# Kernel optimization log

Measured on AMD Instinct MI355X. Metric: run time of the kernel, lower is better.

The kernel has to match this reference:

```python
import jax, jax.numpy as jnp
import numpy as np

N_ELEMS = 200000
N_REACTIONS = 100000
ELEM_DIM = 200
REACT_DIM = 128
N_HEADS = 3
DIMS = [ELEM_DIM + REACT_DIM, 256, 256, 256, 256, 128, 128, 64]  # ResidualNetwork layer dims


def _init(key, shape, fan_in):
    return jax.random.normal(key, shape, dtype=jnp.float32) * (1.0 / np.sqrt(fan_in))


def setup_inputs() -> dict:
    key = jax.random.key(0)
    ks = jax.random.split(key, 32)
    H = N_HEADS
    inp = {
        "orig_elem_fea": jax.random.normal(ks[0], (N_ELEMS, ELEM_DIM), dtype=jnp.float32),
        "reaction_elem_idx": jax.random.randint(ks[1], (N_ELEMS,), 0, N_REACTIONS, dtype=jnp.int32),
        "reaction_embed": jax.random.normal(ks[2], (N_REACTIONS, REACT_DIM), dtype=jnp.float32),
    }
    k = 3
    for i in range(7):
        inp[f"fcW{i}"] = _init(ks[k], (H, DIMS[i], DIMS[i + 1]), DIMS[i]); k += 1
        inp[f"fcb{i}"] = jnp.zeros((H, DIMS[i + 1]), dtype=jnp.float32)
    # residual projections only where in_dim != out_dim (layers 0, 4, 6)
    for i in (0, 4, 6):
        inp[f"resW{i}"] = _init(ks[k], (H, DIMS[i], DIMS[i + 1]), DIMS[i]); k += 1
    inp["outW"] = _init(ks[k], (H, DIMS[-1], 1), DIMS[-1]); k += 1
    inp["outb"] = jnp.zeros((H, 1), dtype=jnp.float32)
    return inp


def reference(orig_elem_fea, reaction_elem_idx, reaction_embed,
              fcW0, fcb0, fcW1, fcb1, fcW2, fcb2, fcW3, fcb3,
              fcW4, fcb4, fcW5, fcb5, fcW6, fcb6,
              resW0, resW4, resW6, outW, outb):
    C = reaction_embed.shape[0]
    idx = reaction_elem_idx
    # gather reaction embedding per elem and concat: (N, E+R)
    fea = jnp.concatenate([orig_elem_fea, reaction_embed[idx]], axis=1)
    # per-head ResidualNetwork gate: h axis = head
    h = jax.nn.relu(jnp.einsum('nf,hfo->hno', fea, fcW0) + fcb0[:, None, :]) \
        + jnp.einsum('nf,hfo->hno', fea, resW0)
    for W, b in ((fcW1, fcb1), (fcW2, fcb2), (fcW3, fcb3)):
        h = jax.nn.relu(jnp.einsum('hnf,hfo->hno', h, W) + b[:, None, :]) + h
    h = jax.nn.relu(jnp.einsum('hnf,hfo->hno', h, fcW4) + fcb4[:, None, :]) \
        + jnp.einsum('hnf,hfo->hno', h, resW4)
    h = jax.nn.relu(jnp.einsum('hnf,hfo->hno', h, fcW5) + fcb5[:, None, :]) + h
    h = jax.nn.relu(jnp.einsum('hnf,hfo->hno', h, fcW6) + fcb6[:, None, :]) \
        + jnp.einsum('hnf,hfo->hno', h, resW6)
    gate = (jnp.einsum('hnf,hfo->hno', h, outW) + outb[:, None, :])[..., 0]  # (H, N)
    # segment softmax over reactions, per head
    seg_max = jax.vmap(lambda g: jax.ops.segment_max(g, idx, num_segments=C))(gate)
    gate = jnp.exp(gate - seg_max[:, idx])
    seg_sum = jax.vmap(lambda g: jax.ops.segment_sum(g, idx, num_segments=C))(gate)
    gate = gate / (seg_sum[:, idx] + 1e-13)
    return jnp.mean(gate, axis=0)  # (N,) normalised stoichiometries
```

## Files before the change

kernel.cpp:

```cpp
#include <hip/hip_runtime.h>

#define NELEM  200000
#define NREACT 100000
#define EDIM   200
#define RDIM   128
#define F0     328
#define F0PAD  352
#define NH     3
#define MT     64
#define NT     256
#define SA     360

typedef _Float16 f16x8 __attribute__((ext_vector_type(8)));
typedef _Float16 f16x4 __attribute__((ext_vector_type(4)));
typedef float    f32x4 __attribute__((ext_vector_type(4)));

struct WSeg { const float* src; _Float16* dst; int K, N, Kpad, nb; };
struct WTab { WSeg s[10]; };

__global__ void wconv_all(WTab t)
{
    __shared__ float sT[64 * 33];
    int b = blockIdx.x;
    for (int i = 0; i < 10; ++i) {
        if (b < t.s[i].nb) {
            const WSeg g = t.s[i];
            const int ntn = 3 * g.N / 64;
            const int tn = b % ntn, tk = b / ntn;
            const int col = tn * 64;
            const int h = col / g.N, n0 = col - h * g.N;
            const int k0 = tk * 32;
            const int tid = threadIdx.x;

            const int nl = tid & 63;
            for (int kk = tid >> 6; kk < 32; kk += 4) {
                const int k = k0 + kk;
                float v = (k < g.K) ? g.src[((size_t)h * g.K + k) * g.N + n0 + nl] : 0.f;
                sT[nl * 33 + kk] = v;
            }
            __syncthreads();

            const int kl = tid & 31;
            for (int nn = tid >> 5; nn < 64; nn += 8)
                g.dst[(size_t)(col + nn) * g.Kpad + k0 + kl] = (_Float16)sT[nn * 33 + kl];
            return;
        }
        b -= t.s[i].nb;
    }
}

template<int TN>
__device__ __forceinline__ void pin_step_refill()
{
    if constexpr (TN == 4) {
#pragma unroll
        for (int g = 0; g < 4; ++g) {
            __builtin_amdgcn_sched_group_barrier(0x008, 2, 0);
            __builtin_amdgcn_sched_group_barrier(0x020, 1, 0);
            __builtin_amdgcn_sched_group_barrier(0x008, 2, 0);
            __builtin_amdgcn_sched_group_barrier(0x100, 1, 0);
        }
    } else if constexpr (TN == 2) {
#pragma unroll
        for (int g = 0; g < 2; ++g) {
            __builtin_amdgcn_sched_group_barrier(0x008, 2, 0);
            __builtin_amdgcn_sched_group_barrier(0x020, 1, 0);
            __builtin_amdgcn_sched_group_barrier(0x008, 2, 0);
            __builtin_amdgcn_sched_group_barrier(0x100, 2, 0);
        }
    } else {
        __builtin_amdgcn_sched_group_barrier(0x008, 2, 0);
        __builtin_amdgcn_sched_group_barrier(0x020, 1, 0);
        __builtin_amdgcn_sched_group_barrier(0x008, 2, 0);
        __builtin_amdgcn_sched_group_barrier(0x100, 4, 0);
    }
}

template<int N>
__device__ __forceinline__ void pin_step_mfma_only()
{
    __builtin_amdgcn_sched_group_barrier(0x008, N, 0);
}

template<int TN, int KSTEPS, int KPAD>
__device__ __forceinline__ void gemm_pass(
    const _Float16* __restrict__ buf,
    const _Float16* __restrict__ w,
    f32x4 (&acc)[4][TN], int n0, int r, int q)
{
    const _Float16* aBase = buf + r * SA + q * 8;
    const _Float16* wBase = w + ((size_t)n0 + r) * KPAD + q * 8;

    f16x8 a0[4], a1[4], b0[TN], b1[TN];
#pragma unroll
    for (int nt = 0; nt < TN; ++nt) b0[nt] = *(const f16x8*)(wBase + (size_t)nt * 16 * KPAD);
#pragma unroll
    for (int mt = 0; mt < 4; ++mt) a0[mt] = *(const f16x8*)(aBase + mt * 16 * SA);
#pragma unroll
    for (int nt = 0; nt < TN; ++nt) b1[nt] = *(const f16x8*)(wBase + (size_t)nt * 16 * KPAD + 32);
#pragma unroll
    for (int mt = 0; mt < 4; ++mt) a1[mt] = *(const f16x8*)(aBase + mt * 16 * SA + 32);

#pragma unroll
    for (int kt = 0; kt < KSTEPS; kt += 2) {
#pragma unroll
        for (int nt = 0; nt < TN; ++nt)
#pragma unroll
            for (int mt = 0; mt < 4; ++mt)
                acc[mt][nt] = __builtin_amdgcn_mfma_f32_16x16x32_f16(b0[nt], a0[mt], acc[mt][nt], 0, 0, 0);
        if (kt + 2 < KSTEPS) {
#pragma unroll
            for (int nt = 0; nt < TN; ++nt)
                b0[nt] = *(const f16x8*)(wBase + (size_t)nt * 16 * KPAD + (kt + 2) * 32);
#pragma unroll
            for (int mt = 0; mt < 4; ++mt)
                a0[mt] = *(const f16x8*)(aBase + mt * 16 * SA + (kt + 2) * 32);
            pin_step_refill<TN>();
        } else {
            pin_step_mfma_only<4 * TN>();
        }
        if (kt + 1 < KSTEPS) {
#pragma unroll
            for (int nt = 0; nt < TN; ++nt)
#pragma unroll
                for (int mt = 0; mt < 4; ++mt)
                    acc[mt][nt] = __builtin_amdgcn_mfma_f32_16x16x32_f16(b1[nt], a1[mt], acc[mt][nt], 0, 0, 0);
            if (kt + 3 < KSTEPS) {
#pragma unroll
                for (int nt = 0; nt < TN; ++nt)
                    b1[nt] = *(const f16x8*)(wBase + (size_t)nt * 16 * KPAD + (kt + 3) * 32);
#pragma unroll
                for (int mt = 0; mt < 4; ++mt)
                    a1[mt] = *(const f16x8*)(aBase + mt * 16 * SA + (kt + 3) * 32);
                pin_step_refill<TN>();
            } else {
                pin_step_mfma_only<4 * TN>();
            }
        }
    }
}

template<int TN, int KSTEPS, int KPAD>
__device__ __forceinline__ void layer_id(
    _Float16* __restrict__ buf,
    const _Float16* __restrict__ wFc,
    const float* __restrict__ bias, int n0, int lane)
{
    const int r = lane & 15, q = lane >> 4;
    f32x4 acc[4][TN];
#pragma unroll
    for (int mt = 0; mt < 4; ++mt)
#pragma unroll
        for (int nt = 0; nt < TN; ++nt) acc[mt][nt] = (f32x4){0.f, 0.f, 0.f, 0.f};

    gemm_pass<TN, KSTEPS, KPAD>(buf, wFc, acc, n0, r, q);

    __syncthreads();

#pragma unroll
    for (int nt = 0; nt < TN; ++nt) {
        const int colb = n0 + nt * 16 + q * 4;
        const f32x4 bv = *(const f32x4*)(bias + colb);
#pragma unroll
        for (int mt = 0; mt < 4; ++mt) {
            _Float16* p = buf + (mt * 16 + r) * SA + colb;
            f16x4 o = *(const f16x4*)p;
            f16x4 z;
#pragma unroll
            for (int i = 0; i < 4; ++i)
                z[i] = (_Float16)(fmaxf(acc[mt][nt][i] + bv[i], 0.f) + (float)o[i]);
            *(f16x4*)p = z;
        }
    }
    __syncthreads();
}

template<int TN, int KSTEPS, int KPAD>
__device__ __forceinline__ void layer_proj(
    _Float16* __restrict__ buf,
    const _Float16* __restrict__ wFc, const _Float16* __restrict__ wRes,
    const float* __restrict__ bias, int n0, int lane)
{
    const int r = lane & 15, q = lane >> 4;
    f32x4 acc[4][TN];
#pragma unroll
    for (int mt = 0; mt < 4; ++mt)
#pragma unroll
        for (int nt = 0; nt < TN; ++nt) acc[mt][nt] = (f32x4){0.f, 0.f, 0.f, 0.f};

    gemm_pass<TN, KSTEPS, KPAD>(buf, wFc, acc, n0, r, q);

#pragma unroll
    for (int nt = 0; nt < TN; ++nt) {
        const f32x4 bv = *(const f32x4*)(bias + n0 + nt * 16 + q * 4);
#pragma unroll
        for (int mt = 0; mt < 4; ++mt)
#pragma unroll
            for (int i = 0; i < 4; ++i)
                acc[mt][nt][i] = fmaxf(acc[mt][nt][i] + bv[i], 0.f);
    }

    gemm_pass<TN, KSTEPS, KPAD>(buf, wRes, acc, n0, r, q);

    __syncthreads();

#pragma unroll
    for (int nt = 0; nt < TN; ++nt) {
        const int colb = n0 + nt * 16 + q * 4;
#pragma unroll
        for (int mt = 0; mt < 4; ++mt) {
            f16x4 z;
#pragma unroll
            for (int i = 0; i < 4; ++i) z[i] = (_Float16)acc[mt][nt][i];
            *(f16x4*)(buf + (mt * 16 + r) * SA + colb) = z;
        }
    }
    __syncthreads();
}

__global__ __launch_bounds__(NT, 3)
void mlp_mfma(const float* __restrict__ elem, const int* __restrict__ ridx,
              const float* __restrict__ embed,
              const _Float16* __restrict__ wb,
              const float* __restrict__ fcb0, const float* __restrict__ fcb1,
              const float* __restrict__ fcb2, const float* __restrict__ fcb3,
              const float* __restrict__ fcb4, const float* __restrict__ fcb5,
              const float* __restrict__ fcb6,
              const float* __restrict__ outW, const float* __restrict__ outb,
              float* __restrict__ gate, unsigned int* __restrict__ segmax)
{
    __shared__ __align__(16) _Float16 sX[MT * SA];
    __shared__ int sidx[MT];

    const int tid = threadIdx.x, lane = tid & 63, wave = tid >> 6;
    const int head = blockIdx.y;
    const int row0 = blockIdx.x * MT;

    if (tid < MT) sidx[tid] = ridx[row0 + tid];
    __syncthreads();

    for (int rr = wave; rr < MT; rr += 4) {
        const float* es = elem + (size_t)(row0 + rr) * EDIM;
        const float* ms = embed + (size_t)sidx[rr] * RDIM;
        for (int c = lane; c < F0PAD / 4; c += 64) {
            f32x4 v;
            if (c < EDIM / 4)            v = *(const f32x4*)(es + 4 * c);
            else if (c < F0 / 4)         v = *(const f32x4*)(ms + 4 * c - EDIM);
            else                         v = (f32x4){0.f, 0.f, 0.f, 0.f};
            f16x4 hv;
#pragma unroll
            for (int i = 0; i < 4; ++i) hv[i] = (_Float16)v[i];
            *(f16x4*)(sX + rr * SA + 4 * c) = hv;
        }
    }
    __syncthreads();

    const size_t h = head;
    const int n64 = wave * 64, n32 = wave * 32, n16 = wave * 16;

    const _Float16* wt_fc0  = wb;
    const _Float16* wt_res0 = wb + 270336;
    const _Float16* wt_fc1  = wb + 540672;
    const _Float16* wt_fc2  = wb + 737280;
    const _Float16* wt_fc3  = wb + 933888;
    const _Float16* wt_fc4  = wb + 1130496;
    const _Float16* wt_res4 = wb + 1228800;
    const _Float16* wt_fc5  = wb + 1327104;
    const _Float16* wt_fc6  = wb + 1376256;
    const _Float16* wt_res6 = wb + 1400832;

    layer_proj<4, 11, 352>(sX, wt_fc0 + h * 90112, wt_res0 + h * 90112, fcb0 + h * 256, n64, lane);
    layer_id  <4, 8, 256>(sX, wt_fc1 + h * 65536, fcb1 + h * 256, n64, lane);
    layer_id  <4, 8, 256>(sX, wt_fc2 + h * 65536, fcb2 + h * 256, n64, lane);
    layer_id  <4, 8, 256>(sX, wt_fc3 + h * 65536, fcb3 + h * 256, n64, lane);
    layer_proj<2, 8, 256>(sX, wt_fc4 + h * 32768, wt_res4 + h * 32768, fcb4 + h * 128, n32, lane);
    layer_id  <2, 4, 128>(sX, wt_fc5 + h * 16384, fcb5 + h * 128, n32, lane);
    layer_proj<1, 4, 128>(sX, wt_fc6 + h * 8192,  wt_res6 + h * 8192,  fcb6 + h * 64,  n16, lane);

    if (tid < MT) {
        const _Float16* hv = sX + tid * SA;
        const float* wv = outW + h * 64;
        float g = outb[head];
#pragma unroll
        for (int j = 0; j < 8; ++j) {
            f16x8 hx = *(const f16x8*)(hv + j * 8);
#pragma unroll
            for (int i = 0; i < 8; ++i) g = fmaf((float)hx[i], wv[j * 8 + i], g);
        }
        gate[head * NELEM + row0 + tid] = g;
        unsigned int bits = __float_as_uint(g);
        unsigned int enc  = (bits & 0x80000000u) ? ~bits : (bits | 0x80000000u);
        atomicMax(&segmax[head * NREACT + sidx[tid]], enc);
    }
}

__global__ void phase2_kernel(float* __restrict__ gate, const int* __restrict__ ridx,
                              const unsigned int* __restrict__ segmax,
                              float* __restrict__ segsum)
{
    int i = blockIdx.x * blockDim.x + threadIdx.x;
    if (i >= NH * NELEM) return;
    int h = i / NELEM;
    int n = i - h * NELEM;
    int j = ridx[n];
    unsigned int enc  = segmax[h * NREACT + j];
    unsigned int bits = (enc & 0x80000000u) ? (enc & 0x7FFFFFFFu) : ~enc;
    float m = __uint_as_float(bits);
    float e = __expf(gate[i] - m);
    gate[i] = e;
    atomicAdd(&segsum[h * NREACT + j], e);
}

__global__ void phase3_kernel(const float* __restrict__ gate, const int* __restrict__ ridx,
                              const float* __restrict__ segsum, float* __restrict__ out)
{
    int n = blockIdx.x * blockDim.x + threadIdx.x;
    if (n >= NELEM) return;
    int j = ridx[n];
    float s = 0.0f;
#pragma unroll
    for (int h = 0; h < NH; ++h)
        s += gate[h * NELEM + n] / (segsum[h * NREACT + j] + 1e-13f);
    out[n] = s * (1.0f / 3.0f);
}

extern "C" void kernel_launch(void* const* d_in, const int* in_sizes, int n_in,
                              void* d_out, int out_size, void* d_ws, size_t ws_size,
                              hipStream_t stream)
{
    const float* elem  = (const float*)d_in[0];
    const int*   ridx  = (const int*)  d_in[1];
    const float* embed = (const float*)d_in[2];
    const float* fcW0  = (const float*)d_in[3];
    const float* fcb0  = (const float*)d_in[4];
    const float* fcW1  = (const float*)d_in[5];
    const float* fcb1  = (const float*)d_in[6];
    const float* fcW2  = (const float*)d_in[7];
    const float* fcb2  = (const float*)d_in[8];
    const float* fcW3  = (const float*)d_in[9];
    const float* fcb3  = (const float*)d_in[10];
    const float* fcW4  = (const float*)d_in[11];
    const float* fcb4  = (const float*)d_in[12];
    const float* fcW5  = (const float*)d_in[13];
    const float* fcb5  = (const float*)d_in[14];
    const float* fcW6  = (const float*)d_in[15];
    const float* fcb6  = (const float*)d_in[16];
    const float* resW0 = (const float*)d_in[17];
    const float* resW4 = (const float*)d_in[18];
    const float* resW6 = (const float*)d_in[19];
    const float* outW  = (const float*)d_in[20];
    const float* outb  = (const float*)d_in[21];

    float*        gate   = (float*)d_ws;
    unsigned int* segmax = (unsigned int*)d_ws + 600000;
    float*        segsum = (float*)d_ws + 900000;
    _Float16*     wbuf   = (_Float16*)((float*)d_ws + 1200000);

    hipMemsetAsync((void*)segmax, 0, sizeof(unsigned int) * 600000, stream);

    WTab t;
    t.s[0] = { fcW0,  wbuf,           328, 256, 352, 132 };
    t.s[1] = { resW0, wbuf + 270336,  328, 256, 352, 132 };
    t.s[2] = { fcW1,  wbuf + 540672,  256, 256, 256,  96 };
    t.s[3] = { fcW2,  wbuf + 737280,  256, 256, 256,  96 };
    t.s[4] = { fcW3,  wbuf + 933888,  256, 256, 256,  96 };
    t.s[5] = { fcW4,  wbuf + 1130496, 256, 128, 256,  48 };
    t.s[6] = { resW4, wbuf + 1228800, 256, 128, 256,  48 };
    t.s[7] = { fcW5,  wbuf + 1327104, 128, 128, 128,  24 };
    t.s[8] = { fcW6,  wbuf + 1376256, 128,  64, 128,  12 };
    t.s[9] = { resW6, wbuf + 1400832, 128,  64, 128,  12 };
    wconv_all<<<696, 256, 0, stream>>>(t);

    dim3 grid(NELEM / MT, NH);
    mlp_mfma<<<grid, NT, 0, stream>>>(elem, ridx, embed, wbuf,
                                      fcb0, fcb1, fcb2, fcb3, fcb4, fcb5, fcb6,
                                      outW, outb, gate, segmax);

    int tot = NH * NELEM;
    phase2_kernel<<<(tot + 255) / 256, 256, 0, stream>>>(gate, ridx, segmax, segsum);
    phase3_kernel<<<(NELEM + 255) / 256, 256, 0, stream>>>(gate, ridx, segsum, (float*)d_out);
}
```

Measured before the change: 1.361 ms.

## Use eight waves per block splitting output columns more finely

Doubles the block to 512 threads so each wave computes half as many output columns per layer (TN halved). The last 64-wide layer gates the extra waves off while keeping them at the block barriers. The aim is more waves resident per CU to hide load latency. In exchange, each A fragment read from LDS is reused across fewer MFMAs, so LDS traffic per FLOP roughly doubles, and the launch bounds now ask for 6 blocks of 512 threads, which tightens register limits.

```diff
diff --git a/kernel.cpp b/kernel.cpp
--- a/kernel.cpp
+++ b/kernel.cpp
@@ -8,7 +8,7 @@
 #define F0PAD  352
 #define NH     3
 #define MT     64
-#define NT     256
+#define NT     512
 #define SA     360
 
 typedef _Float16 f16x8 __attribute__((ext_vector_type(8)));
@@ -52,15 +52,7 @@
 template<int TN>
 __device__ __forceinline__ void pin_step_refill()
 {
-    if constexpr (TN == 4) {
-#pragma unroll
-        for (int g = 0; g < 4; ++g) {
-            __builtin_amdgcn_sched_group_barrier(0x008, 2, 0);
-            __builtin_amdgcn_sched_group_barrier(0x020, 1, 0);
-            __builtin_amdgcn_sched_group_barrier(0x008, 2, 0);
-            __builtin_amdgcn_sched_group_barrier(0x100, 1, 0);
-        }
-    } else if constexpr (TN == 2) {
+    if constexpr (TN == 2) {
 #pragma unroll
         for (int g = 0; g < 2; ++g) {
             __builtin_amdgcn_sched_group_barrier(0x008, 2, 0);
@@ -142,34 +134,37 @@
 
 template<int TN, int KSTEPS, int KPAD>
 __device__ __forceinline__ void layer_id(
-    _Float16* __restrict__ buf,
+    bool active, _Float16* __restrict__ buf,
     const _Float16* __restrict__ wFc,
     const float* __restrict__ bias, int n0, int lane)
 {
     const int r = lane & 15, q = lane >> 4;
     f32x4 acc[4][TN];
-#pragma unroll
-    for (int mt = 0; mt < 4; ++mt)
-#pragma unroll
-        for (int nt = 0; nt < TN; ++nt) acc[mt][nt] = (f32x4){0.f, 0.f, 0.f, 0.f};
-
-    gemm_pass<TN, KSTEPS, KPAD>(buf, wFc, acc, n0, r, q);
-
-    __syncthreads();
-
-#pragma unroll
-    for (int nt = 0; nt < TN; ++nt) {
-        const int colb = n0 + nt * 16 + q * 4;
-        const f32x4 bv = *(const f32x4*)(bias + colb);
-#pragma unroll
-        for (int mt = 0; mt < 4; ++mt) {
-            _Float16* p = buf + (mt * 16 + r) * SA + colb;
-            f16x4 o = *(const f16x4*)p;
-            f16x4 z;
-#pragma unroll
-            for (int i = 0; i < 4; ++i)
-                z[i] = (_Float16)(fmaxf(acc[mt][nt][i] + bv[i], 0.f) + (float)o[i]);
-            *(f16x4*)p = z;
+    if (active) {
+#pragma unroll
+        for (int mt = 0; mt < 4; ++mt)
+#pragma unroll
+            for (int nt = 0; nt < TN; ++nt) acc[mt][nt] = (f32x4){0.f, 0.f, 0.f, 0.f};
+        gemm_pass<TN, KSTEPS, KPAD>(buf, wFc, acc, n0, r, q);
+    }
+
+    __syncthreads();
+
+    if (active) {
+#pragma unroll
+        for (int nt = 0; nt < TN; ++nt) {
+            const int colb = n0 + nt * 16 + q * 4;
+            const f32x4 bv = *(const f32x4*)(bias + colb);
+#pragma unroll
+            for (int mt = 0; mt < 4; ++mt) {
+                _Float16* p = buf + (mt * 16 + r) * SA + colb;
+                f16x4 o = *(const f16x4*)p;
+                f16x4 z;
+#pragma unroll
+                for (int i = 0; i < 4; ++i)
+                    z[i] = (_Float16)(fmaxf(acc[mt][nt][i] + bv[i], 0.f) + (float)o[i]);
+                *(f16x4*)p = z;
+            }
         }
     }
     __syncthreads();
@@ -177,48 +172,52 @@
 
 template<int TN, int KSTEPS, int KPAD>
 __device__ __forceinline__ void layer_proj(
-    _Float16* __restrict__ buf,
+    bool active, _Float16* __restrict__ buf,
     const _Float16* __restrict__ wFc, const _Float16* __restrict__ wRes,
     const float* __restrict__ bias, int n0, int lane)
 {
     const int r = lane & 15, q = lane >> 4;
     f32x4 acc[4][TN];
-#pragma unroll
-    for (int mt = 0; mt < 4; ++mt)
-#pragma unroll
-        for (int nt = 0; nt < TN; ++nt) acc[mt][nt] = (f32x4){0.f, 0.f, 0.f, 0.f};
-
-    gemm_pass<TN, KSTEPS, KPAD>(buf, wFc, acc, n0, r, q);
-
-#pragma unroll
-    for (int nt = 0; nt < TN; ++nt) {
-        const f32x4 bv = *(const f32x4*)(bias + n0 + nt * 16 + q * 4);
+    if (active) {
 #pragma unroll
         for (int mt = 0; mt < 4; ++mt)
 #pragma unroll
-            for (int i = 0; i < 4; ++i)
-                acc[mt][nt][i] = fmaxf(acc[mt][nt][i] + bv[i], 0.f);
-    }
-
-    gemm_pass<TN, KSTEPS, KPAD>(buf, wRes, acc, n0, r, q);
-
-    __syncthreads();
-
-#pragma unroll
-    for (int nt = 0; nt < TN; ++nt) {
-        const int colb = n0 + nt * 16 + q * 4;
-#pragma unroll
-        for (int mt = 0; mt < 4; ++mt) {
-            f16x4 z;
-#pragma unroll
-            for (int i = 0; i < 4; ++i) z[i] = (_Float16)acc[mt][nt][i];
-            *(f16x4*)(buf + (mt * 16 + r) * SA + colb) = z;
-        }
-    }
-    __syncthreads();
-}
-
-__global__ __launch_bounds__(NT, 3)
+            for (int nt = 0; nt < TN; ++nt) acc[mt][nt] = (f32x4){0.f, 0.f, 0.f, 0.f};
+
+        gemm_pass<TN, KSTEPS, KPAD>(buf, wFc, acc, n0, r, q);
+
+#pragma unroll
+        for (int nt = 0; nt < TN; ++nt) {
+            const f32x4 bv = *(const f32x4*)(bias + n0 + nt * 16 + q * 4);
+#pragma unroll
+            for (int mt = 0; mt < 4; ++mt)
+#pragma unroll
+                for (int i = 0; i < 4; ++i)
+                    acc[mt][nt][i] = fmaxf(acc[mt][nt][i] + bv[i], 0.f);
+        }
+
+        gemm_pass<TN, KSTEPS, KPAD>(buf, wRes, acc, n0, r, q);
+    }
+
+    __syncthreads();
+
+    if (active) {
+#pragma unroll
+        for (int nt = 0; nt < TN; ++nt) {
+            const int colb = n0 + nt * 16 + q * 4;
+#pragma unroll
+            for (int mt = 0; mt < 4; ++mt) {
+                f16x4 z;
+#pragma unroll
+                for (int i = 0; i < 4; ++i) z[i] = (_Float16)acc[mt][nt][i];
+                *(f16x4*)(buf + (mt * 16 + r) * SA + colb) = z;
+            }
+        }
+    }
+    __syncthreads();
+}
+
+__global__ __launch_bounds__(NT, 6)
 void mlp_mfma(const float* __restrict__ elem, const int* __restrict__ ridx,
               const float* __restrict__ embed,
               const _Float16* __restrict__ wb,
@@ -239,7 +238,7 @@
     if (tid < MT) sidx[tid] = ridx[row0 + tid];
     __syncthreads();
 
-    for (int rr = wave; rr < MT; rr += 4) {
+    for (int rr = wave; rr < MT; rr += 8) {
         const float* es = elem + (size_t)(row0 + rr) * EDIM;
         const float* ms = embed + (size_t)sidx[rr] * RDIM;
         for (int c = lane; c < F0PAD / 4; c += 64) {
@@ -256,7 +255,7 @@
     __syncthreads();
 
     const size_t h = head;
-    const int n64 = wave * 64, n32 = wave * 32, n16 = wave * 16;
+    const int n32 = wave * 32, n16 = wave * 16;
 
     const _Float16* wt_fc0  = wb;
     const _Float16* wt_res0 = wb + 270336;
@@ -269,13 +268,13 @@
     const _Float16* wt_fc6  = wb + 1376256;
     const _Float16* wt_res6 = wb + 1400832;
 
-    layer_proj<4, 11, 352>(sX, wt_fc0 + h * 90112, wt_res0 + h * 90112, fcb0 + h * 256, n64, lane);
-    layer_id  <4, 8, 256>(sX, wt_fc1 + h * 65536, fcb1 + h * 256, n64, lane);
-    layer_id  <4, 8, 256>(sX, wt_fc2 + h * 65536, fcb2 + h * 256, n64, lane);
-    layer_id  <4, 8, 256>(sX, wt_fc3 + h * 65536, fcb3 + h * 256, n64, lane);
-    layer_proj<2, 8, 256>(sX, wt_fc4 + h * 32768, wt_res4 + h * 32768, fcb4 + h * 128, n32, lane);
-    layer_id  <2, 4, 128>(sX, wt_fc5 + h * 16384, fcb5 + h * 128, n32, lane);
-    layer_proj<1, 4, 128>(sX, wt_fc6 + h * 8192,  wt_res6 + h * 8192,  fcb6 + h * 64,  n16, lane);
+    layer_proj<2, 11, 352>(true, sX, wt_fc0 + h * 90112, wt_res0 + h * 90112, fcb0 + h * 256, n32, lane);
+    layer_id  <2, 8, 256>(true, sX, wt_fc1 + h * 65536, fcb1 + h * 256, n32, lane);
+    layer_id  <2, 8, 256>(true, sX, wt_fc2 + h * 65536, fcb2 + h * 256, n32, lane);
+    layer_id  <2, 8, 256>(true, sX, wt_fc3 + h * 65536, fcb3 + h * 256, n32, lane);
+    layer_proj<1, 8, 256>(true, sX, wt_fc4 + h * 32768, wt_res4 + h * 32768, fcb4 + h * 128, n16, lane);
+    layer_id  <1, 4, 128>(true, sX, wt_fc5 + h * 16384, fcb5 + h * 128, n16, lane);
+    layer_proj<1, 4, 128>(wave < 4, sX, wt_fc6 + h * 8192, wt_res6 + h * 8192, fcb6 + h * 64, n16, lane);
 
     if (tid < MT) {
         const _Float16* hv = sX + tid * SA;
```

New measurement: 3.494 ms. 157% more time.
